# Kernel tuning notes

Hardware: AMD Instinct MI355X
Metric: run time of the kernel (lower is better)

Reference implementation:

```python
import jax, jax.numpy as jnp
import numpy as np

B, H, D = 16, 32, 128          # batch, heads, head_dim
NB, BS, MB = 1024, 16, 128     # num cache blocks, block_size, max blocks per seq
HIDDEN = H * D
EPS = 1e-6


def setup_inputs() -> dict:
    key = jax.random.key(0)
    ks = jax.random.split(key, 5)
    return {
        "hidden_states": jax.random.normal(ks[0], (B, HIDDEN), dtype=jnp.float32),
        "key_cache": jax.random.normal(ks[1], (NB, BS, H, D), dtype=jnp.float32),
        "value_cache": jax.random.normal(ks[2], (NB, BS, H, D), dtype=jnp.float32),
        "block_tables": jax.random.randint(ks[3], (B, MB), 0, NB, dtype=jnp.int32),
        "context_lens": jax.random.randint(ks[4], (B,), 1, MB * BS + 1, dtype=jnp.int32),
        "rms_weight": jnp.ones((HIDDEN,), dtype=jnp.float32),
    }


def reference(hidden_states, key_cache, value_cache, block_tables, context_lens, rms_weight):
    bsz = hidden_states.shape[0]
    nb, bs, h, d = key_cache.shape
    scale = 1.0 / np.sqrt(d).astype(np.float32)

    residual = hidden_states
    # RMSNorm
    x = hidden_states
    norm = x * jax.lax.rsqrt(jnp.mean(x * x, axis=-1, keepdims=True) + EPS) * rms_weight
    q = norm.reshape(bsz, h, d)  # [B, H, D] single decode token per sequence

    # Paged KV gather: block_tables [B, MB] indexes into cache blocks
    keys = key_cache[block_tables].reshape(bsz, -1, h, d)    # [B, S, H, D], S = MB*BS
    vals = value_cache[block_tables].reshape(bsz, -1, h, d)  # [B, S, H, D]
    s = keys.shape[1]

    scores = jnp.einsum('bhd,bshd->bhs', q, keys) * scale    # [B, H, S]
    valid = jnp.arange(s, dtype=jnp.int32)[None, :] < context_lens[:, None]  # [B, S]
    scores = jnp.where(valid[:, None, :], scores, -jnp.inf)
    probs = jax.nn.softmax(scores, axis=-1)
    attn = jnp.einsum('bhs,bshd->bhd', probs, vals).reshape(bsz, h * d)

    return residual + attn
```

## Files before the change

kernel.cpp:

```cpp
#include <hip/hip_runtime.h>
#include <math.h>

#define BATCH 16
#define NHEAD 32
#define HDIM 128
#define HIDDEN 4096
#define BS 16
#define MB 128
#define EPS 1e-6f
#define SPLIT 128

#define PCOUNT (BATCH * NHEAD * SPLIT)
#define PL_OFF PCOUNT
#define PA_OFF (2 * PCOUNT)

__global__ __launch_bounds__(256) void attn_page_kernel(
    const float* __restrict__ x, const float* __restrict__ rw,
    const float* __restrict__ kc, const float* __restrict__ vc,
    const int* __restrict__ bt, const int* __restrict__ cl,
    float* __restrict__ pm, float* __restrict__ pl, float* __restrict__ pacc) {
    const int si = blockIdx.x;
    const int b = blockIdx.y;
    const int L = cl[b];
    const int nsp = (L + BS - 1) >> 4;
    if (si >= nsp) return;
    const int nt = min(BS, L - (si << 4));
    const int tid = threadIdx.x;
    const int hw = tid >> 5;
    const int lane = tid & 31;

    const float4* xr = (const float4*)(x + (size_t)b * HIDDEN);
    const float4* wr = (const float4*)rw;
    float4 qf[4];
    float ss = 0.f;
#pragma unroll
    for (int i = 0; i < 4; i++) {
        float4 v = xr[tid + 256 * i];
        qf[i] = v;
        ss += v.x * v.x + v.y * v.y + v.z * v.z + v.w * v.w;
    }
#pragma unroll
    for (int m = 32; m >= 1; m >>= 1) ss += __shfl_xor(ss, m, 64);
    __shared__ float red[4];
    if ((tid & 63) == 0) red[tid >> 6] = ss;
    __syncthreads();
    const float rstd = rsqrtf((red[0] + red[1] + red[2] + red[3]) * (1.0f / HIDDEN) + EPS);
#pragma unroll
    for (int i = 0; i < 4; i++) {
        float4 wv = wr[tid + 256 * i];
        qf[i].x *= rstd * wv.x;
        qf[i].y *= rstd * wv.y;
        qf[i].z *= rstd * wv.z;
        qf[i].w *= rstd * wv.w;
    }

    const int pg = bt[b * MB + si];
    const float4* kb = (const float4*)(kc + (size_t)pg * (BS * HIDDEN));
    const float4* vb = (const float4*)(vc + (size_t)pg * (BS * HIDDEN));

    const float scale = 0.08838834764831845f;
    float m0[4], l0[4];
    float4 acc[4];
#pragma unroll
    for (int i = 0; i < 4; i++) {
        m0[i] = -INFINITY;
        l0[i] = 0.f;
        acc[i] = make_float4(0.f, 0.f, 0.f, 0.f);
    }

    for (int t = 0; t < nt; ++t) {
        const float4* krow = kb + (size_t)t * (HIDDEN / 4);
        const float4* vrow = vb + (size_t)t * (HIDDEN / 4);
        float4 k4[4], v4[4];
#pragma unroll
        for (int i = 0; i < 4; i++) {
            k4[i] = krow[tid + 256 * i];
            v4[i] = vrow[tid + 256 * i];
        }
#pragma unroll
        for (int i = 0; i < 4; i++) {
            float d = k4[i].x * qf[i].x + k4[i].y * qf[i].y + k4[i].z * qf[i].z +
                      k4[i].w * qf[i].w;
#pragma unroll
            for (int msk = 16; msk >= 1; msk >>= 1) d += __shfl_xor(d, msk, 64);
            float sc = d * scale;
            float mn = fmaxf(m0[i], sc);
            float al = __expf(m0[i] - mn);
            float p = __expf(sc - mn);
            l0[i] = l0[i] * al + p;
            acc[i].x = acc[i].x * al + p * v4[i].x;
            acc[i].y = acc[i].y * al + p * v4[i].y;
            acc[i].z = acc[i].z * al + p * v4[i].z;
            acc[i].w = acc[i].w * al + p * v4[i].w;
            m0[i] = mn;
        }
    }

#pragma unroll
    for (int i = 0; i < 4; i++) {
        const int h = hw + 8 * i;
        const size_t pb = (size_t)(b * NHEAD + h) * SPLIT + si;
        if (lane == 0) {
            pm[pb] = m0[i];
            pl[pb] = l0[i];
        }
        *(float4*)(pacc + pb * HDIM + 4 * lane) = acc[i];
    }
}

__global__ __launch_bounds__(128) void attn_combine_kernel(
    const float* __restrict__ pm, const float* __restrict__ pl,
    const float* __restrict__ pacc, const float* __restrict__ resid,
    const int* __restrict__ cl, float* __restrict__ out) {
    const int h = blockIdx.x;
    const int b = blockIdx.y;
    const int tid = threadIdx.x;
    const int L = cl[b];
    const int nsp = (L + BS - 1) >> 4;
    const size_t pb0 = (size_t)(b * NHEAD + h) * SPLIT;

    float M = -INFINITY;
    for (int si = 0; si < nsp; ++si) M = fmaxf(M, pm[pb0 + si]);
    float Ls = 0.f, A = 0.f;
#pragma unroll 4
    for (int si = 0; si < nsp; ++si) {
        float sc = __expf(pm[pb0 + si] - M);
        Ls += pl[pb0 + si] * sc;
        A += pacc[(pb0 + si) * HDIM + tid] * sc;
    }
    const size_t oi = (size_t)b * HIDDEN + h * HDIM + tid;
    out[oi] = resid[oi] + A / Ls;
}

extern "C" void kernel_launch(void* const* d_in, const int* in_sizes, int n_in,
                              void* d_out, int out_size, void* d_ws, size_t ws_size,
                              hipStream_t stream) {
    const float* hs = (const float*)d_in[0];
    const float* kc = (const float*)d_in[1];
    const float* vc = (const float*)d_in[2];
    const int* bt = (const int*)d_in[3];
    const int* cl = (const int*)d_in[4];
    const float* rw = (const float*)d_in[5];
    float* out = (float*)d_out;
    float* ws = (float*)d_ws;
    float* pm = ws;
    float* pl = ws + PL_OFF;
    float* pacc = ws + PA_OFF;

    attn_page_kernel<<<dim3(SPLIT, BATCH), 256, 0, stream>>>(hs, rw, kc, vc, bt, cl,
                                                             pm, pl, pacc);
    attn_combine_kernel<<<dim3(NHEAD, BATCH), 128, 0, stream>>>(pm, pl, pacc, hs, cl, out);
}
```

Baseline: 513.0 us.

## Split pages into half-chunks, double-buffer KV loads, parallelize combine reduction

```diff
diff --git a/kernel.cpp b/kernel.cpp
--- a/kernel.cpp
+++ b/kernel.cpp
@@ -8,13 +8,43 @@
 #define BS 16
 #define MB 128
 #define EPS 1e-6f
-#define SPLIT 128
+#define CHUNK 8
+#define SPLIT 256
+
+typedef float floatx4 __attribute__((ext_vector_type(4)));
 
 #define PCOUNT (BATCH * NHEAD * SPLIT)
 #define PL_OFF PCOUNT
 #define PA_OFF (2 * PCOUNT)
 
-__global__ __launch_bounds__(256) void attn_page_kernel(
+#define LOADKV(KA, VA, T)                                                       \
+    do {                                                                        \
+        const floatx4* kr_ = kbp + (size_t)(T) * (HIDDEN / 4);                  \
+        const floatx4* vr_ = vbp + (size_t)(T) * (HIDDEN / 4);                  \
+        _Pragma("unroll") for (int i_ = 0; i_ < 4; i_++) {                      \
+            KA[i_] = __builtin_nontemporal_load(&kr_[tid + 256 * i_]);          \
+            VA[i_] = __builtin_nontemporal_load(&vr_[tid + 256 * i_]);          \
+        }                                                                       \
+    } while (0)
+
+#define COMPUTE(KA, VA)                                                         \
+    do {                                                                        \
+        _Pragma("unroll") for (int i_ = 0; i_ < 4; i_++) {                      \
+            float d_ = KA[i_][0] * qf[i_][0] + KA[i_][1] * qf[i_][1] +          \
+                       KA[i_][2] * qf[i_][2] + KA[i_][3] * qf[i_][3];           \
+            _Pragma("unroll") for (int msk_ = 16; msk_ >= 1; msk_ >>= 1)        \
+                d_ += __shfl_xor(d_, msk_, 64);                                 \
+            float sc_ = d_ * 0.08838834764831845f;                              \
+            float mn_ = fmaxf(m0[i_], sc_);                                     \
+            float al_ = __expf(m0[i_] - mn_);                                   \
+            float p_ = __expf(sc_ - mn_);                                       \
+            l0[i_] = l0[i_] * al_ + p_;                                         \
+            acc[i_] = acc[i_] * al_ + p_ * VA[i_];                              \
+            m0[i_] = mn_;                                                       \
+        }                                                                       \
+    } while (0)
+
+__global__ __launch_bounds__(256, 4) void attn_page_kernel(
     const float* __restrict__ x, const float* __restrict__ rw,
     const float* __restrict__ kc, const float* __restrict__ vc,
     const int* __restrict__ bt, const int* __restrict__ cl,
@@ -22,22 +52,22 @@
     const int si = blockIdx.x;
     const int b = blockIdx.y;
     const int L = cl[b];
-    const int nsp = (L + BS - 1) >> 4;
+    const int nsp = (L + CHUNK - 1) >> 3;
     if (si >= nsp) return;
-    const int nt = min(BS, L - (si << 4));
+    const int nt = min(CHUNK, L - (si << 3));
     const int tid = threadIdx.x;
     const int hw = tid >> 5;
     const int lane = tid & 31;
 
-    const float4* xr = (const float4*)(x + (size_t)b * HIDDEN);
-    const float4* wr = (const float4*)rw;
-    float4 qf[4];
+    const floatx4* xr = (const floatx4*)(x + (size_t)b * HIDDEN);
+    const floatx4* wr = (const floatx4*)rw;
+    floatx4 qf[4];
     float ss = 0.f;
 #pragma unroll
     for (int i = 0; i < 4; i++) {
-        float4 v = xr[tid + 256 * i];
+        floatx4 v = xr[tid + 256 * i];
         qf[i] = v;
-        ss += v.x * v.x + v.y * v.y + v.z * v.z + v.w * v.w;
+        ss += v[0] * v[0] + v[1] * v[1] + v[2] * v[2] + v[3] * v[3];
     }
 #pragma unroll
     for (int m = 32; m >= 1; m >>= 1) ss += __shfl_xor(ss, m, 64);
@@ -47,52 +77,41 @@
     const float rstd = rsqrtf((red[0] + red[1] + red[2] + red[3]) * (1.0f / HIDDEN) + EPS);
 #pragma unroll
     for (int i = 0; i < 4; i++) {
-        float4 wv = wr[tid + 256 * i];
-        qf[i].x *= rstd * wv.x;
-        qf[i].y *= rstd * wv.y;
-        qf[i].z *= rstd * wv.z;
-        qf[i].w *= rstd * wv.w;
-    }
-
-    const int pg = bt[b * MB + si];
-    const float4* kb = (const float4*)(kc + (size_t)pg * (BS * HIDDEN));
-    const float4* vb = (const float4*)(vc + (size_t)pg * (BS * HIDDEN));
-
-    const float scale = 0.08838834764831845f;
+        floatx4 wv = wr[tid + 256 * i];
+        qf[i] *= rstd * wv;
+    }
+
+    const int pg = bt[b * MB + (si >> 1)];
+    const int t0 = (si & 1) * CHUNK;
+    const floatx4* kbp = (const floatx4*)(kc + (size_t)pg * (BS * HIDDEN)) +
+                         (size_t)t0 * (HIDDEN / 4);
+    const floatx4* vbp = (const floatx4*)(vc + (size_t)pg * (BS * HIDDEN)) +
+                         (size_t)t0 * (HIDDEN / 4);
+
     float m0[4], l0[4];
-    float4 acc[4];
+    floatx4 acc[4];
 #pragma unroll
     for (int i = 0; i < 4; i++) {
         m0[i] = -INFINITY;
         l0[i] = 0.f;
-        acc[i] = make_float4(0.f, 0.f, 0.f, 0.f);
-    }
-
-    for (int t = 0; t < nt; ++t) {
-        const float4* krow = kb + (size_t)t * (HIDDEN / 4);
-        const float4* vrow = vb + (size_t)t * (HIDDEN / 4);
-        float4 k4[4], v4[4];
-#pragma unroll
-        for (int i = 0; i < 4; i++) {
-            k4[i] = krow[tid + 256 * i];
-            v4[i] = vrow[tid + 256 * i];
+        acc[i] = (floatx4)(0.f);
+    }
+
+    if (nt == CHUNK) {
+        floatx4 kA[4], vA[4], kB[4], vB[4];
+        LOADKV(kA, vA, 0);
+#pragma unroll
+        for (int t = 0; t < CHUNK; t += 2) {
+            LOADKV(kB, vB, t + 1);
+            COMPUTE(kA, vA);
+            if (t + 2 < CHUNK) LOADKV(kA, vA, t + 2);
+            COMPUTE(kB, vB);
         }
-#pragma unroll
-        for (int i = 0; i < 4; i++) {
-            float d = k4[i].x * qf[i].x + k4[i].y * qf[i].y + k4[i].z * qf[i].z +
-                      k4[i].w * qf[i].w;
-#pragma unroll
-            for (int msk = 16; msk >= 1; msk >>= 1) d += __shfl_xor(d, msk, 64);
-            float sc = d * scale;
-            float mn = fmaxf(m0[i], sc);
-            float al = __expf(m0[i] - mn);
-            float p = __expf(sc - mn);
-            l0[i] = l0[i] * al + p;
-            acc[i].x = acc[i].x * al + p * v4[i].x;
-            acc[i].y = acc[i].y * al + p * v4[i].y;
-            acc[i].z = acc[i].z * al + p * v4[i].z;
-            acc[i].w = acc[i].w * al + p * v4[i].w;
-            m0[i] = mn;
+    } else {
+        for (int t = 0; t < nt; ++t) {
+            floatx4 k4[4], v4[4];
+            LOADKV(k4, v4, t);
+            COMPUTE(k4, v4);
         }
     }
 
@@ -104,7 +123,7 @@
             pm[pb] = m0[i];
             pl[pb] = l0[i];
         }
-        *(float4*)(pacc + pb * HDIM + 4 * lane) = acc[i];
+        *(floatx4*)(pacc + pb * HDIM + 4 * lane) = acc[i];
     }
 }
 
@@ -116,18 +135,49 @@
     const int b = blockIdx.y;
     const int tid = threadIdx.x;
     const int L = cl[b];
-    const int nsp = (L + BS - 1) >> 4;
+    const int nsp = (L + CHUNK - 1) >> 3;
     const size_t pb0 = (size_t)(b * NHEAD + h) * SPLIT;
 
-    float M = -INFINITY;
-    for (int si = 0; si < nsp; ++si) M = fmaxf(M, pm[pb0 + si]);
-    float Ls = 0.f, A = 0.f;
-#pragma unroll 4
-    for (int si = 0; si < nsp; ++si) {
-        float sc = __expf(pm[pb0 + si] - M);
-        Ls += pl[pb0 + si] * sc;
-        A += pacc[(pb0 + si) * HDIM + tid] * sc;
-    }
+    __shared__ float s_w[SPLIT];
+    __shared__ float s_red[2];
+    __shared__ float s_red2[2];
+
+    const float m0v = (tid < nsp) ? pm[pb0 + tid] : -INFINITY;
+    const float m1v = (tid + 128 < nsp) ? pm[pb0 + tid + 128] : -INFINITY;
+    float mx = fmaxf(m0v, m1v);
+#pragma unroll
+    for (int msk = 32; msk >= 1; msk >>= 1) mx = fmaxf(mx, __shfl_xor(mx, msk, 64));
+    if ((tid & 63) == 0) s_red[tid >> 6] = mx;
+    __syncthreads();
+    const float M = fmaxf(s_red[0], s_red[1]);
+
+    float lsum = 0.f;
+    if (tid < nsp) {
+        float w = __expf(m0v - M);
+        s_w[tid] = w;
+        lsum += pl[pb0 + tid] * w;
+    }
+    if (tid + 128 < nsp) {
+        float w = __expf(m1v - M);
+        s_w[tid + 128] = w;
+        lsum += pl[pb0 + tid + 128] * w;
+    }
+#pragma unroll
+    for (int msk = 32; msk >= 1; msk >>= 1) lsum += __shfl_xor(lsum, msk, 64);
+    if ((tid & 63) == 0) s_red2[tid >> 6] = lsum;
+    __syncthreads();
+    const float Ls = s_red2[0] + s_red2[1];
+
+    float A = 0.f;
+    const float* pa = pacc + pb0 * HDIM + tid;
+    int si = 0;
+    for (; si + 4 <= nsp; si += 4) {
+        A += s_w[si] * pa[(size_t)si * HDIM] + s_w[si + 1] * pa[(size_t)(si + 1) * HDIM] +
+             s_w[si + 2] * pa[(size_t)(si + 2) * HDIM] +
+             s_w[si + 3] * pa[(size_t)(si + 3) * HDIM];
+    }
+    for (; si < nsp; ++si) A += s_w[si] * pa[(size_t)si * HDIM];
+
     const size_t oi = (size_t)b * HIDDEN + h * HDIM + tid;
     out[oi] = resid[oi] + A / Ls;
 }
```

After: 518.1 us. About the same (+1.0%).
